# Kernel tuning notes

Hardware: AMD Instinct MI355X
Metric: run time of the kernel (lower is better)

Reference implementation:

```python
import jax, jax.numpy as jnp
import numpy as np

D_IN, D_OUT, K = 128, 256, 16
B, N = 2, 16384
D_HALF = D_OUT // 2
EPS = 1e-6
GROUPS = 16


def conv1x1(x, w, b):
    # x: (B,C,N,K), w: (O,C), b: (O,)
    return jnp.einsum('oc,bcnk->bonk', w, x) + b[None, :, None, None]


def groupnorm(x, w, b, groups=GROUPS):
    Bv, C, Nv, Kv = x.shape
    xr = x.reshape(Bv, groups, C // groups, Nv, Kv)
    m = xr.mean(axis=(2, 3, 4), keepdims=True)
    v = xr.var(axis=(2, 3, 4), keepdims=True)
    xn = ((xr - m) / jnp.sqrt(v + EPS)).reshape(Bv, C, Nv, Kv)
    return xn * w[None, :, None, None] + b[None, :, None, None]


def lse(coords, x, idx, dist, w, b, gw, gb):
    # coords: (B,N,3); x: (B,C,N,1); idx: (B,N,K); dist: (B,N,K)
    nbr = jax.vmap(lambda c, i: c[i])(coords, idx)          # (B,N,K,3)
    ctr = jnp.broadcast_to(coords[:, :, None, :], nbr.shape)  # (B,N,K,3)
    rel = jnp.concatenate([ctr, nbr, ctr - nbr], axis=-1)    # (B,N,K,9)
    geo = jnp.concatenate([rel.transpose(0, 3, 1, 2), dist[:, None, :, :]], axis=1)  # (B,10,N,K)
    geo = jax.nn.relu(groupnorm(conv1x1(geo, w, b), gw, gb))  # (B,d/2,N,K)
    nf = jax.vmap(lambda f, i: f[:, i])(x[..., 0], idx)       # (B,d/2,N,K)
    return jnp.concatenate([geo, nf], axis=1)                 # (B,d,N,K)


def attentive_pool(x, w, b, gw, gb):
    m = x.mean(axis=-1, keepdims=True)  # (B,C,N,1)
    return jax.nn.relu(groupnorm(conv1x1(m, w, b), gw, gb))


def setup_inputs() -> dict:
    key = jax.random.key(0)
    ks = jax.random.split(key, 16)
    s = 0.02
    d = {
        'coords': jax.random.normal(ks[0], (B, N, 3), jnp.float32),
        'features': jax.random.normal(ks[1], (B, D_IN, N, 1), jnp.float32),
        'knn_dist': jax.random.uniform(ks[2], (B, N, K), jnp.float32),
        'knn_idx': jax.random.randint(ks[3], (B, N, K), 0, N),
        'w1': jax.random.normal(ks[4], (D_HALF, D_IN), jnp.float32) * s,
        'b1': jnp.zeros((D_HALF,), jnp.float32),
        'lse1_w': jax.random.normal(ks[5], (D_HALF, 10), jnp.float32) * s,
        'lse1_b': jnp.zeros((D_HALF,), jnp.float32),
        'lse1_gw': jnp.ones((D_HALF,), jnp.float32),
        'lse1_gb': jnp.zeros((D_HALF,), jnp.float32),
        'pool1_w': jax.random.normal(ks[6], (D_HALF, D_OUT), jnp.float32) * s,
        'pool1_b': jnp.zeros((D_HALF,), jnp.float32),
        'pool1_gw': jnp.ones((D_HALF,), jnp.float32),
        'pool1_gb': jnp.zeros((D_HALF,), jnp.float32),
        'lse2_w': jax.random.normal(ks[7], (D_HALF, 10), jnp.float32) * s,
        'lse2_b': jnp.zeros((D_HALF,), jnp.float32),
        'lse2_gw': jnp.ones((D_HALF,), jnp.float32),
        'lse2_gb': jnp.zeros((D_HALF,), jnp.float32),
        'pool2_w': jax.random.normal(ks[8], (D_OUT, D_OUT), jnp.float32) * s,
        'pool2_b': jnp.zeros((D_OUT,), jnp.float32),
        'pool2_gw': jnp.ones((D_OUT,), jnp.float32),
        'pool2_gb': jnp.zeros((D_OUT,), jnp.float32),
        'mlp2_w': jax.random.normal(ks[9], (2 * D_OUT, D_OUT), jnp.float32) * s,
        'mlp2_b': jnp.zeros((2 * D_OUT,), jnp.float32),
        'sc_w': jax.random.normal(ks[10], (2 * D_OUT, D_IN), jnp.float32) * s,
        'sc_b': jnp.zeros((2 * D_OUT,), jnp.float32),
        'sc_gw': jnp.ones((2 * D_OUT,), jnp.float32),
        'sc_gb': jnp.zeros((2 * D_OUT,), jnp.float32),
    }
    return d


def reference(coords, features, knn_dist, knn_idx,
              w1, b1,
              lse1_w, lse1_b, lse1_gw, lse1_gb,
              pool1_w, pool1_b, pool1_gw, pool1_gb,
              lse2_w, lse2_b, lse2_gw, lse2_gb,
              pool2_w, pool2_b, pool2_gw, pool2_gb,
              mlp2_w, mlp2_b, sc_w, sc_b, sc_gw, sc_gb):
    # mlp1: conv + LeakyReLU(0.2), no norm
    x = jax.nn.leaky_relu(conv1x1(features, w1, b1), 0.2)        # (B,d/2,N,1)
    x = lse(coords, x, knn_idx, knn_dist, lse1_w, lse1_b, lse1_gw, lse1_gb)  # (B,d,N,K)
    x = attentive_pool(x, pool1_w, pool1_b, pool1_gw, pool1_gb)  # (B,d/2,N,1)
    x = lse(coords, x, knn_idx, knn_dist, lse2_w, lse2_b, lse2_gw, lse2_gb)  # (B,d,N,K)
    x = attentive_pool(x, pool2_w, pool2_b, pool2_gw, pool2_gb)  # (B,d,N,1)
    main = conv1x1(x, mlp2_w, mlp2_b)                            # (B,2d,N,1)
    short = groupnorm(conv1x1(features, sc_w, sc_b), sc_gw, sc_gb)
    return jax.nn.leaky_relu(main + short, 0.01)                 # (B,2d,N,1)
```

## Files before the change

### kernel.cpp

```cpp
#include <hip/hip_runtime.h>


constexpr int Bc = 2;
constexpr int Nc = 16384;
constexpr int Kc = 16;
constexpr float EPSc = 1e-6f;

typedef __attribute__((ext_vector_type(8))) short short8;
typedef __attribute__((ext_vector_type(4))) short short4v;
typedef __attribute__((ext_vector_type(4))) float floatx4;

__device__ inline short f2bf(float x) {
    union { float f; unsigned u; } v; v.f = x;
    unsigned r = v.u + 0x7fffu + ((v.u >> 16) & 1u);
    return (short)(r >> 16);
}
__device__ inline float bf2f(short s) {
    union { unsigned u; float f; } v;
    v.u = ((unsigned)(unsigned short)s) << 16;
    return v.f;
}

constexpr size_t OW_W1  = 0;
constexpr size_t OW_P1W = OW_W1  + 128*128;
constexpr size_t OW_P2W = OW_P1W + 128*256;
constexpr size_t OW_M2W = OW_P2W + 256*256;
constexpr size_t OW_SCW = OW_M2W + 512*256;
constexpr size_t OW_L1W = OW_SCW + 512*128;
constexpr size_t OW_L2W = OW_L1W + 128*32;
constexpr size_t OW_FB  = OW_L2W + 128*32;
constexpr size_t OW_X1  = OW_FB  + (size_t)Bc*Nc*128;
constexpr size_t OW_M   = OW_X1  + (size_t)Bc*Nc*128;
constexpr size_t OW_Z1  = OW_M   + (size_t)Bc*Nc*256;
constexpr size_t OW_Z2  = OW_Z1  + (size_t)Bc*Nc*128;
constexpr size_t OW_S   = OW_Z2  + (size_t)Bc*Nc*256;

constexpr int CV0 = 128*128;
constexpr int CV1 = CV0 + 128*256;
constexpr int CV2 = CV1 + 256*256;
constexpr int CV3 = CV2 + 512*256;
constexpr int CV4 = CV3 + 512*128;
constexpr int CV5 = CV4 + 128*32;
constexpr int CV6 = CV5 + 128*32;
constexpr int CVTOT = CV6 + 1024;

__global__ void prep_kernel(const float* __restrict__ w1,
                            const float* __restrict__ p1w,
                            const float* __restrict__ p2w,
                            const float* __restrict__ m2w,
                            const float* __restrict__ scw,
                            const float* __restrict__ l1w,
                            const float* __restrict__ l2w,
                            short* __restrict__ W16,
                            float* __restrict__ ST)
{
    int i = blockIdx.x * 256 + threadIdx.x;
    if (i < CV0) { W16[OW_W1  + i] = f2bf(w1[i]); return; }
    if (i < CV1) { int k = i - CV0; W16[OW_P1W + k] = f2bf(p1w[k]); return; }
    if (i < CV2) { int k = i - CV1; W16[OW_P2W + k] = f2bf(p2w[k]); return; }
    if (i < CV3) { int k = i - CV2; W16[OW_M2W + k] = f2bf(m2w[k]); return; }
    if (i < CV4) { int k = i - CV3; W16[OW_SCW + k] = f2bf(scw[k]); return; }
    if (i < CV5) { int k = i - CV4; int o = k >> 5, c = k & 31;
                   W16[OW_L1W + k] = (c < 10) ? f2bf(l1w[o*10+c]) : (short)0; return; }
    if (i < CV6) { int k = i - CV5; int o = k >> 5, c = k & 31;
                   W16[OW_L2W + k] = (c < 10) ? f2bf(l2w[o*10+c]) : (short)0; return; }
    { int k = i - CV6; if (k < 1024) ST[k] = 0.f; }
}

__global__ void feat_t_kernel(const float* __restrict__ in, short* __restrict__ out) {
    int tid  = threadIdx.x;
    int lane = tid & 63, wave = tid >> 6;
    int bb = blockIdx.x / (Nc / 64);
    int n  = (blockIdx.x % (Nc / 64)) * 64 + lane;
    #pragma unroll
    for (int cc = 0; cc < 4; cc++) {
        int c0 = (wave + cc * 4) * 8;
        short8 sv;
        #pragma unroll
        for (int i = 0; i < 8; i++)
            sv[i] = f2bf(in[((size_t)bb * 128 + c0 + i) * Nc + n]);
        *(short8*)&out[((size_t)(bb * Nc + n)) * 128 + c0] = sv;
    }
}

__launch_bounds__(256)
__global__ void geo_reduce_kernel(const float* __restrict__ coords,
                                  const int* __restrict__ knn_idx,
                                  const float* __restrict__ knn_dist,
                                  float* __restrict__ dst)
{
    __shared__ float part[4][65];
    const int tid  = threadIdx.x;
    const int b    = blockIdx.y;
    const int base = blockIdx.x * 256 + tid;
    const float* cb  = coords   + (size_t)b * Nc * 3;
    const int*   ib  = knn_idx  + (size_t)b * Nc * Kc;
    const float* db  = knn_dist + (size_t)b * Nc * Kc;

    float acc[65];
    #pragma unroll
    for (int i = 0; i < 65; i++) acc[i] = 0.f;

    #pragma unroll
    for (int it = 0; it < 4; it++) {
        int r = base + it * 65536;
        int n = r >> 4;
        float cx = cb[n*3+0], cy = cb[n*3+1], cz = cb[n*3+2];
        int   j  = ib[r];
        float nx = cb[j*3+0], ny = cb[j*3+1], nz = cb[j*3+2];
        float d  = db[r];
        float g[10] = {cx,cy,cz,nx,ny,nz,cx-nx,cy-ny,cz-nz,d};
        #pragma unroll
        for (int c = 0; c < 10; c++) acc[c] += g[c];
        int idx = 10;
        #pragma unroll
        for (int c = 0; c < 10; c++)
            #pragma unroll
            for (int c2 = c; c2 < 10; c2++) acc[idx++] += g[c] * g[c2];
    }
    #pragma unroll
    for (int i = 0; i < 65; i++) {
        float v = acc[i];
        #pragma unroll
        for (int off = 1; off < 64; off <<= 1) v += __shfl_xor(v, off);
        acc[i] = v;
    }
    int lane = tid & 63, wave = tid >> 6;
    if (lane == 0) {
        #pragma unroll
        for (int i = 0; i < 65; i++) part[wave][i] = acc[i];
    }
    __syncthreads();
    if (tid < 65) {
        float s = part[0][tid] + part[1][tid] + part[2][tid] + part[3][tid];
        atomicAdd(&dst[b * 65 + tid], s);
    }
}

template<int CIN, int COUT, int GROUP_CH, int MODE>
__launch_bounds__(256)
__global__ void gemm_conv(const short* __restrict__ wA,
                          const short* __restrict__ xB,
                          const float* __restrict__ bias,
                          short* __restrict__ outb,
                          float* __restrict__ outf,
                          float* __restrict__ stats,
                          const short* __restrict__ sbuf,
                          const float* __restrict__ st_sc,
                          const float* __restrict__ gw,
                          const float* __restrict__ gb,
                          float sc_cnt,
                          const float* __restrict__ bst,
                          const float* __restrict__ bgw,
                          const float* __restrict__ bgb,
                          float bcnt)
{
    __shared__ short Abuf[128 * 40];
    __shared__ short Bbuf[128 * 40];
    __shared__ float sstat[32];
    __shared__ float smean[4], sinv[4];
    __shared__ float bsc[256], bsh[256];

    const int tid  = threadIdx.x;
    const int n0   = blockIdx.x * 128;
    const int mo   = blockIdx.y * 128;
    const int b    = blockIdx.z;
    const int lane = tid & 63;
    const int wave = tid >> 6;
    const int wm   = (wave >> 1) * 64;
    const int wn   = (wave & 1) * 64;
    const int l15  = lane & 15;
    const int quad = lane >> 4;

    if constexpr (MODE == 2) { if (tid < 32) sstat[tid] = 0.f; }
    if constexpr (MODE == 3) {
        if (tid < 4) {
            int g = (mo >> 5) + tid;
            float s0 = st_sc[(b * 16 + g) * 2 + 0];
            float s1 = st_sc[(b * 16 + g) * 2 + 1];
            float mean = s0 / sc_cnt;
            float var  = s1 / sc_cnt - mean * mean;
            smean[tid] = mean;
            sinv[tid]  = rsqrtf(var + EPSc);
        }
        if (tid < CIN) {
            int g = tid >> 4;
            float s0 = bst[(b * 16 + g) * 2 + 0];
            float s1 = bst[(b * 16 + g) * 2 + 1];
            float mean = s0 / bcnt;
            float var  = s1 / bcnt - mean * mean;
            float inv  = rsqrtf(var + EPSc);
            float sc_  = inv * bgw[tid];
            bsc[tid] = sc_;
            bsh[tid] = bgb[tid] - mean * sc_;
        }
    }

    floatx4 acc[4][4];
    #pragma unroll
    for (int mi = 0; mi < 4; mi++)
        #pragma unroll
        for (int ni = 0; ni < 4; ni++)
            acc[mi][ni] = (floatx4){0.f, 0.f, 0.f, 0.f};

    const short* wAr = wA + (size_t)mo * CIN;
    const short* xBr = xB + (size_t)b * Nc * CIN + (size_t)n0 * CIN;

    for (int c0 = 0; c0 < CIN; c0 += 32) {
        __syncthreads();
        #pragma unroll
        for (int s = 0; s < 2; s++) {
            int e = tid + s * 256;
            int r = e >> 2, q = e & 3;
            *(short8*)&Abuf[r * 40 + q * 8] =
                *(const short8*)(wAr + (size_t)r * CIN + c0 + q * 8);
            short8 v = *(const short8*)(xBr + (size_t)r * CIN + c0 + q * 8);
            if constexpr (MODE == 3) {
                #pragma unroll
                for (int i = 0; i < 8; i++) {
                    int ch = c0 + q * 8 + i;
                    float t = bf2f(v[i]) * bsc[ch] + bsh[ch];
                    v[i] = f2bf(t > 0.f ? t : 0.f);
                }
            }
            *(short8*)&Bbuf[r * 40 + q * 8] = v;
        }
        __syncthreads();

        short8 af[4], bfr[4];
        #pragma unroll
        for (int mi = 0; mi < 4; mi++)
            af[mi] = *(short8*)&Abuf[(wm + mi * 16 + l15) * 40 + quad * 8];
        #pragma unroll
        for (int ni = 0; ni < 4; ni++)
            bfr[ni] = *(short8*)&Bbuf[(wn + ni * 16 + l15) * 40 + quad * 8];
        #pragma unroll
        for (int mi = 0; mi < 4; mi++)
            #pragma unroll
            for (int ni = 0; ni < 4; ni++)
                acc[mi][ni] = __builtin_amdgcn_mfma_f32_16x16x32_bf16(
                    af[mi], bfr[ni], acc[mi][ni], 0, 0, 0);
    }

    #pragma unroll
    for (int mi = 0; mi < 4; mi++) {
        int rowl = wm + mi * 16 + quad * 4;
        float b4[4], gw4[4], gb4[4];
        #pragma unroll
        for (int r = 0; r < 4; r++) {
            b4[r] = bias[mo + rowl + r];
            if constexpr (MODE == 3) {
                gw4[r] = gw[mo + rowl + r];
                gb4[r] = gb[mo + rowl + r];
            }
        }
        float gs = 0.f, gq = 0.f;
        #pragma unroll
        for (int ni = 0; ni < 4; ni++) {
            int col = n0 + wn + ni * 16 + l15;
            if constexpr (MODE == 3) {
                short4v s4 = *(const short4v*)&sbuf[((size_t)(b * Nc + col)) * 512 + mo + rowl];
                int gl = rowl >> 5;
                #pragma unroll
                for (int r = 0; r < 4; r++) {
                    float v = acc[mi][ni][r] + b4[r];
                    float s = bf2f(s4[r]);
                    float sn = (s - smean[gl]) * sinv[gl] * gw4[r] + gb4[r];
                    float o = v + sn;
                    o = o > 0.f ? o : 0.01f * o;
                    outf[((size_t)b * COUT + mo + rowl + r) * Nc + col] = o;
                }
            } else {
                short4v sv;
                #pragma unroll
                for (int r = 0; r < 4; r++) {
                    float v = acc[mi][ni][r] + b4[r];
                    if constexpr (MODE == 1) v = v > 0.f ? v : 0.2f * v;
                    if constexpr (MODE == 2) { gs += v; gq += v * v; }
                    sv[r] = f2bf(v);
                }
                *(short4v*)&outb[((size_t)(b * Nc + col)) * COUT + mo + rowl] = sv;
            }
        }
        if constexpr (MODE == 2) {
            #pragma unroll
            for (int off = 1; off < 16; off <<= 1) {
                gs += __shfl_xor(gs, off);
                gq += __shfl_xor(gq, off);
            }
            if (l15 == 0) {
                int gl = rowl / GROUP_CH;
                atomicAdd(&sstat[gl * 2 + 0], gs);
                atomicAdd(&sstat[gl * 2 + 1], gq);
            }
        }
    }
    if constexpr (MODE == 2) {
        __syncthreads();
        constexpr int NG = 128 / GROUP_CH;
        if (tid < 2 * NG) {
            int g0 = mo / GROUP_CH;
            atomicAdd(&stats[b * 32 + (g0 + (tid >> 1)) * 2 + (tid & 1)], sstat[tid]);
        }
    }
}

__launch_bounds__(256)
__global__ void lse_m_kernel(const float* __restrict__ coords,
                             const int* __restrict__ knn_idx,
                             const float* __restrict__ knn_dist,
                             const short* __restrict__ xprev,
                             const short* __restrict__ wpad,
                             const float* __restrict__ wf,
                             const float* __restrict__ bias,
                             const float* __restrict__ gw,
                             const float* __restrict__ gb,
                             const float* __restrict__ geoS,
                             const float* __restrict__ xst,
                             const float* __restrict__ xgw,
                             const float* __restrict__ xgb,
                             float xcnt,
                             short* __restrict__ m)
{
    __shared__ short Abuf[128 * 40];
    __shared__ short Bbuf[256 * 40];
    __shared__ int   jl[256];
    __shared__ float osum[128], osq[128];
    __shared__ float smean[16], sinv[16];
    __shared__ float xscs[128], xshs[128];

    const int tid = threadIdx.x;
    const int b   = blockIdx.x >> 10;
    const int n0  = (blockIdx.x & 1023) * 16;
    const float NK = (float)(Nc * Kc);
    const bool norm = (xst != nullptr);

    {
        int* bz = (int*)Bbuf;
        #pragma unroll
        for (int i = 0; i < 20; i++) bz[tid + i * 256] = 0;
    }
    #pragma unroll
    for (int s = 0; s < 2; s++) {
        int e = tid + s * 256;
        int o = e >> 2, q = e & 3;
        *(short8*)&Abuf[o * 40 + q * 8] = *(const short8*)(wpad + o * 32 + q * 8);
    }
    if (tid < 128) {
        const float* S = geoS + b * 65;
        float w[10];
        #pragma unroll
        for (int c = 0; c < 10; c++) w[c] = wf[tid * 10 + c];
        float wS = 0.f;
        #pragma unroll
        for (int c = 0; c < 10; c++) wS += w[c] * S[c];
        float q = 0.f;
        {
            int idx = 10;
            #pragma unroll
            for (int c = 0; c < 10; c++)
                #pragma unroll
                for (int c2 = c; c2 < 10; c2++) {
                    float t = w[c] * w[c2] * S[idx++];
                    q += (c == c2) ? t : 2.f * t;
                }
        }
        float bo = bias[tid];
        osum[tid] = NK * bo + wS;
        osq[tid]  = NK * bo * bo + 2.f * bo * wS + q;
        if (norm) {
            int g = tid >> 3;
            float s0 = xst[(b * 16 + g) * 2 + 0];
            float s1 = xst[(b * 16 + g) * 2 + 1];
            float mean = s0 / xcnt;
            float var  = s1 / xcnt - mean * mean;
            float inv  = rsqrtf(var + EPSc);
            float sc_  = inv * xgw[tid];
            xscs[tid] = sc_;
            xshs[tid] = xgb[tid] - mean * sc_;
        }
    }
    __syncthreads();

    {
        int pt = tid & 15, k = tid >> 4;
        int n  = n0 + pt;
        const float* cb = coords + (size_t)b * Nc * 3;
        float cx = cb[n*3+0], cy = cb[n*3+1], cz = cb[n*3+2];
        int   j  = knn_idx[((size_t)b * Nc + n) * Kc + k];
        float nx = cb[j*3+0], ny = cb[j*3+1], nz = cb[j*3+2];
        float d  = knn_dist[((size_t)b * Nc + n) * Kc + k];
        float g[10] = {cx,cy,cz,nx,ny,nz,cx-nx,cy-ny,cz-nz,d};
        int col = k * 16 + pt;
        #pragma unroll
        for (int c = 0; c < 10; c++) Bbuf[col * 40 + c] = f2bf(g[c]);
        jl[col] = j;
    }
    __syncthreads();
    if (tid < 16) {
        float s = 0.f, q = 0.f;
        #pragma unroll
        for (int i = 0; i < 8; i++) { s += osum[tid * 8 + i]; q += osq[tid * 8 + i]; }
        float cnt  = 8.f * NK;
        float mean = s / cnt;
        float var  = q / cnt - mean * mean;
        smean[tid] = mean;
        sinv[tid]  = rsqrtf(var + EPSc);
    }
    __syncthreads();

    const int lane = tid & 63, wave = tid >> 6;
    const int l15 = lane & 15, quad = lane >> 4;
    short8 bfr[16];
    #pragma unroll
    for (int ni = 0; ni < 16; ni++)
        bfr[ni] = *(short8*)&Bbuf[(ni * 16 + l15) * 40 + quad * 8];
    #pragma unroll
    for (int mt2 = 0; mt2 < 2; mt2++) {
        int mt = wave * 2 + mt2;
        short8 af = *(short8*)&Abuf[(mt * 16 + l15) * 40 + quad * 8];
        floatx4 acc[16];
        #pragma unroll
        for (int ni = 0; ni < 16; ni++) {
            acc[ni] = (floatx4){0.f, 0.f, 0.f, 0.f};
            acc[ni] = __builtin_amdgcn_mfma_f32_16x16x32_bf16(af, bfr[ni], acc[ni], 0, 0, 0);
        }
        short4v sv;
        #pragma unroll
        for (int r = 0; r < 4; r++) {
            int o = mt * 16 + quad * 4 + r;
            int g = o >> 3;
            float mu = smean[g], iv = sinv[g];
            float bo = bias[o], gwo = gw[o], gbo = gb[o];
            float s = 0.f;
            #pragma unroll
            for (int ni = 0; ni < 16; ni++) {
                float v = (acc[ni][r] + bo - mu) * iv * gwo + gbo;
                s += v > 0.f ? v : 0.f;
            }
            sv[r] = f2bf(s * (1.f / 16.f));
        }
        *(short4v*)&m[((size_t)(b * Nc + n0 + l15)) * 256 + mt * 16 + quad * 4] = sv;
    }

    {
        int tp = tid & 15, cs = tid >> 4;
        float sc8[8], sh8[8];
        if (norm) {
            #pragma unroll
            for (int i = 0; i < 8; i++) { sc8[i] = xscs[cs*8+i]; sh8[i] = xshs[cs*8+i]; }
        }
        float acc8[8];
        #pragma unroll
        for (int i = 0; i < 8; i++) acc8[i] = 0.f;
        #pragma unroll
        for (int k = 0; k < 16; k++) {
            int j = jl[k * 16 + tp];
            short8 v = *(const short8*)&xprev[((size_t)(b * Nc + j)) * 128 + cs * 8];
            if (norm) {
                #pragma unroll
                for (int i = 0; i < 8; i++) {
                    float t = bf2f(v[i]) * sc8[i] + sh8[i];
                    acc8[i] += t > 0.f ? t : 0.f;
                }
            } else {
                #pragma unroll
                for (int i = 0; i < 8; i++) acc8[i] += bf2f(v[i]);
            }
        }
        short8 sv;
        #pragma unroll
        for (int i = 0; i < 8; i++) sv[i] = f2bf(acc8[i] * (1.f / 16.f));
        *(short8*)&m[((size_t)(b * Nc + n0 + tp)) * 256 + 128 + cs * 8] = sv;
    }
}

extern "C" void kernel_launch(void* const* d_in, const int* in_sizes, int n_in,
                              void* d_out, int out_size, void* d_ws, size_t ws_size,
                              hipStream_t stream)
{
    const float* coords   = (const float*)d_in[0];
    const float* features = (const float*)d_in[1];
    const float* knn_dist = (const float*)d_in[2];
    const int*   knn_idx  = (const int*)  d_in[3];
    const float* w1       = (const float*)d_in[4];
    const float* b1       = (const float*)d_in[5];
    const float* lse1_w   = (const float*)d_in[6];
    const float* lse1_b   = (const float*)d_in[7];
    const float* lse1_gw  = (const float*)d_in[8];
    const float* lse1_gb  = (const float*)d_in[9];
    const float* pool1_w  = (const float*)d_in[10];
    const float* pool1_b  = (const float*)d_in[11];
    const float* pool1_gw = (const float*)d_in[12];
    const float* pool1_gb = (const float*)d_in[13];
    const float* lse2_w   = (const float*)d_in[14];
    const float* lse2_b   = (const float*)d_in[15];
    const float* lse2_gw  = (const float*)d_in[16];
    const float* lse2_gb  = (const float*)d_in[17];
    const float* pool2_w  = (const float*)d_in[18];
    const float* pool2_b  = (const float*)d_in[19];
    const float* pool2_gw = (const float*)d_in[20];
    const float* pool2_gb = (const float*)d_in[21];
    const float* mlp2_w   = (const float*)d_in[22];
    const float* mlp2_b   = (const float*)d_in[23];
    const float* sc_w     = (const float*)d_in[24];
    const float* sc_b     = (const float*)d_in[25];
    const float* sc_gw    = (const float*)d_in[26];
    const float* sc_gb    = (const float*)d_in[27];
    (void)in_sizes; (void)n_in; (void)out_size; (void)ws_size;

    float* ST = (float*)d_ws;
    float* ST_SC  = ST + 0;
    float* ST_P1  = ST + 64;
    float* ST_P2  = ST + 128;
    float* ST_GEO = ST + 256;
    short* W16 = (short*)(ST + 1024);
    short* W1b  = W16 + OW_W1;
    short* P1Wb = W16 + OW_P1W;
    short* P2Wb = W16 + OW_P2W;
    short* M2Wb = W16 + OW_M2W;
    short* SCWb = W16 + OW_SCW;
    short* L1Wb = W16 + OW_L1W;
    short* L2Wb = W16 + OW_L2W;
    short* FB   = W16 + OW_FB;
    short* X1B  = W16 + OW_X1;
    short* MB   = W16 + OW_M;
    short* Z1   = W16 + OW_Z1;
    short* Z2   = W16 + OW_Z2;
    short* SB   = W16 + OW_S;
    float* out  = (float*)d_out;

    prep_kernel<<<(CVTOT + 255) / 256, 256, 0, stream>>>(
        w1, pool1_w, pool2_w, mlp2_w, sc_w, lse1_w, lse2_w, W16, ST);
    feat_t_kernel<<<Bc * Nc / 64, 256, 0, stream>>>(features, FB);
    geo_reduce_kernel<<<dim3(256, Bc), 256, 0, stream>>>(
        coords, knn_idx, knn_dist, ST_GEO);

    gemm_conv<128,512,32,2><<<dim3(Nc/128, 4, Bc), 256, 0, stream>>>(
        SCWb, FB, sc_b, SB, nullptr, ST_SC, nullptr, nullptr, nullptr, nullptr, 0.f,
        nullptr, nullptr, nullptr, 0.f);
    gemm_conv<128,128,8,1><<<dim3(Nc/128, 1, Bc), 256, 0, stream>>>(
        W1b, FB, b1, X1B, nullptr, nullptr, nullptr, nullptr, nullptr, nullptr, 0.f,
        nullptr, nullptr, nullptr, 0.f);
    lse_m_kernel<<<Bc * Nc / 16, 256, 0, stream>>>(
        coords, knn_idx, knn_dist, X1B, L1Wb, lse1_w, lse1_b, lse1_gw, lse1_gb,
        ST_GEO, nullptr, nullptr, nullptr, 0.f, MB);
    gemm_conv<256,128,8,2><<<dim3(Nc/128, 1, Bc), 256, 0, stream>>>(
        P1Wb, MB, pool1_b, Z1, nullptr, ST_P1, nullptr, nullptr, nullptr, nullptr, 0.f,
        nullptr, nullptr, nullptr, 0.f);
    lse_m_kernel<<<Bc * Nc / 16, 256, 0, stream>>>(
        coords, knn_idx, knn_dist, Z1, L2Wb, lse2_w, lse2_b, lse2_gw, lse2_gb,
        ST_GEO, ST_P1, pool1_gw, pool1_gb, (float)(8 * Nc), MB);
    gemm_conv<256,256,16,2><<<dim3(Nc/128, 2, Bc), 256, 0, stream>>>(
        P2Wb, MB, pool2_b, Z2, nullptr, ST_P2, nullptr, nullptr, nullptr, nullptr, 0.f,
        nullptr, nullptr, nullptr, 0.f);
    gemm_conv<256,512,32,3><<<dim3(Nc/128, 4, Bc), 256, 0, stream>>>(
        M2Wb, Z2, mlp2_b, nullptr, out, nullptr, SB, ST_SC, sc_gw, sc_gb,
        (float)(32 * Nc), ST_P2, pool2_gw, pool2_gb, (float)(16 * Nc));
}
```

Baseline: 350.1 us.

## Fuse attentive-pool conv into LSE kernel, keeping pooled features in LDS

The LSE kernel now keeps each 16-point tile's pooled features (256 channels) in shared memory and runs the pool 1x1 conv with MFMA in the same kernel. It writes the pool output and its groupnorm statistics directly, and the two separate pool GEMM launches are removed. This avoids writing and re-reading the intermediate M buffer and saves two launches. In exchange, pool weights are read from global memory by every 16-point block with no LDS staging and with low reuse per block, and the lse weight tile is also read from global memory instead of LDS.

```diff
diff --git a/kernel.cpp b/kernel.cpp
--- a/kernel.cpp
+++ b/kernel.cpp
@@ -30,8 +30,7 @@
 constexpr size_t OW_L2W = OW_L1W + 128*32;
 constexpr size_t OW_FB  = OW_L2W + 128*32;
 constexpr size_t OW_X1  = OW_FB  + (size_t)Bc*Nc*128;
-constexpr size_t OW_M   = OW_X1  + (size_t)Bc*Nc*128;
-constexpr size_t OW_Z1  = OW_M   + (size_t)Bc*Nc*256;
+constexpr size_t OW_Z1  = OW_X1  + (size_t)Bc*Nc*128;
 constexpr size_t OW_Z2  = OW_Z1  + (size_t)Bc*Nc*128;
 constexpr size_t OW_S   = OW_Z2  + (size_t)Bc*Nc*256;
 
@@ -305,29 +304,34 @@
     }
 }
 
+template<int POOL_COUT, int PGROUP>
 __launch_bounds__(256)
-__global__ void lse_m_kernel(const float* __restrict__ coords,
-                             const int* __restrict__ knn_idx,
-                             const float* __restrict__ knn_dist,
-                             const short* __restrict__ xprev,
-                             const short* __restrict__ wpad,
-                             const float* __restrict__ wf,
-                             const float* __restrict__ bias,
-                             const float* __restrict__ gw,
-                             const float* __restrict__ gb,
-                             const float* __restrict__ geoS,
-                             const float* __restrict__ xst,
-                             const float* __restrict__ xgw,
-                             const float* __restrict__ xgb,
-                             float xcnt,
-                             short* __restrict__ m)
+__global__ void lse_pool_kernel(const float* __restrict__ coords,
+                                const int* __restrict__ knn_idx,
+                                const float* __restrict__ knn_dist,
+                                const short* __restrict__ xprev,
+                                const short* __restrict__ wpad,
+                                const float* __restrict__ wf,
+                                const float* __restrict__ gbias,
+                                const float* __restrict__ ggw,
+                                const float* __restrict__ ggb,
+                                const float* __restrict__ geoS,
+                                const float* __restrict__ xst,
+                                const float* __restrict__ xgw,
+                                const float* __restrict__ xgb,
+                                float xcnt,
+                                const short* __restrict__ pw,
+                                const float* __restrict__ pbias,
+                                float* __restrict__ pstats,
+                                short* __restrict__ z)
 {
-    __shared__ short Abuf[128 * 40];
     __shared__ short Bbuf[256 * 40];
+    __shared__ short Mbuf[16 * 264];
     __shared__ int   jl[256];
     __shared__ float osum[128], osq[128];
     __shared__ float smean[16], sinv[16];
     __shared__ float xscs[128], xshs[128];
+    __shared__ float sstat[32];
 
     const int tid = threadIdx.x;
     const int b   = blockIdx.x >> 10;
@@ -335,16 +339,11 @@
     const float NK = (float)(Nc * Kc);
     const bool norm = (xst != nullptr);
 
+    if (tid < 32) sstat[tid] = 0.f;
     {
         int* bz = (int*)Bbuf;
         #pragma unroll
         for (int i = 0; i < 20; i++) bz[tid + i * 256] = 0;
-    }
-    #pragma unroll
-    for (int s = 0; s < 2; s++) {
-        int e = tid + s * 256;
-        int o = e >> 2, q = e & 3;
-        *(short8*)&Abuf[o * 40 + q * 8] = *(const short8*)(wpad + o * 32 + q * 8);
     }
     if (tid < 128) {
         const float* S = geoS + b * 65;
@@ -365,7 +364,7 @@
                     q += (c == c2) ? t : 2.f * t;
                 }
         }
-        float bo = bias[tid];
+        float bo = gbias[tid];
         osum[tid] = NK * bo + wS;
         osq[tid]  = NK * bo * bo + 2.f * bo * wS + q;
         if (norm) {
@@ -418,7 +417,7 @@
     #pragma unroll
     for (int mt2 = 0; mt2 < 2; mt2++) {
         int mt = wave * 2 + mt2;
-        short8 af = *(short8*)&Abuf[(mt * 16 + l15) * 40 + quad * 8];
+        short8 af = *(const short8*)(wpad + (mt * 16 + l15) * 32 + quad * 8);
         floatx4 acc[16];
         #pragma unroll
         for (int ni = 0; ni < 16; ni++) {
@@ -431,7 +430,7 @@
             int o = mt * 16 + quad * 4 + r;
             int g = o >> 3;
             float mu = smean[g], iv = sinv[g];
-            float bo = bias[o], gwo = gw[o], gbo = gb[o];
+            float bo = gbias[o], gwo = ggw[o], gbo = ggb[o];
             float s = 0.f;
             #pragma unroll
             for (int ni = 0; ni < 16; ni++) {
@@ -440,7 +439,7 @@
             }
             sv[r] = f2bf(s * (1.f / 16.f));
         }
-        *(short4v*)&m[((size_t)(b * Nc + n0 + l15)) * 256 + mt * 16 + quad * 4] = sv;
+        *(short4v*)&Mbuf[l15 * 264 + mt * 16 + quad * 4] = sv;
     }
 
     {
@@ -471,8 +470,50 @@
         short8 sv;
         #pragma unroll
         for (int i = 0; i < 8; i++) sv[i] = f2bf(acc8[i] * (1.f / 16.f));
-        *(short8*)&m[((size_t)(b * Nc + n0 + tp)) * 256 + 128 + cs * 8] = sv;
-    }
+        *(short8*)&Mbuf[tp * 264 + 128 + cs * 8] = sv;
+    }
+    __syncthreads();
+
+    constexpr int MTW = POOL_COUT / 64;
+    floatx4 pacc[MTW];
+    #pragma unroll
+    for (int mi = 0; mi < MTW; mi++) pacc[mi] = (floatx4){0.f, 0.f, 0.f, 0.f};
+    #pragma unroll
+    for (int kc = 0; kc < 8; kc++) {
+        short8 bfp = *(short8*)&Mbuf[l15 * 264 + kc * 32 + quad * 8];
+        #pragma unroll
+        for (int mi = 0; mi < MTW; mi++) {
+            int mt = wave * MTW + mi;
+            short8 afp = *(const short8*)(pw + (size_t)(mt * 16 + l15) * 256 + kc * 32 + quad * 8);
+            pacc[mi] = __builtin_amdgcn_mfma_f32_16x16x32_bf16(afp, bfp, pacc[mi], 0, 0, 0);
+        }
+    }
+    #pragma unroll
+    for (int mi = 0; mi < MTW; mi++) {
+        int mt = wave * MTW + mi;
+        float gs = 0.f, gq = 0.f;
+        short4v sv;
+        #pragma unroll
+        for (int r = 0; r < 4; r++) {
+            int o = mt * 16 + quad * 4 + r;
+            float v = pacc[mi][r] + pbias[o];
+            gs += v; gq += v * v;
+            sv[r] = f2bf(v);
+        }
+        *(short4v*)&z[((size_t)(b * Nc + n0 + l15)) * POOL_COUT + mt * 16 + quad * 4] = sv;
+        #pragma unroll
+        for (int off = 1; off < 16; off <<= 1) {
+            gs += __shfl_xor(gs, off);
+            gq += __shfl_xor(gq, off);
+        }
+        if (l15 == 0) {
+            int g = (mt * 16 + quad * 4) / PGROUP;
+            atomicAdd(&sstat[g * 2 + 0], gs);
+            atomicAdd(&sstat[g * 2 + 1], gq);
+        }
+    }
+    __syncthreads();
+    if (tid < 32) atomicAdd(&pstats[b * 32 + tid], sstat[tid]);
 }
 
 extern "C" void kernel_launch(void* const* d_in, const int* in_sizes, int n_in,
@@ -524,7 +565,6 @@
     short* L2Wb = W16 + OW_L2W;
     short* FB   = W16 + OW_FB;
     short* X1B  = W16 + OW_X1;
-    short* MB   = W16 + OW_M;
     short* Z1   = W16 + OW_Z1;
     short* Z2   = W16 + OW_Z2;
     short* SB   = W16 + OW_S;
@@ -542,18 +582,12 @@
     gemm_conv<128,128,8,1><<<dim3(Nc/128, 1, Bc), 256, 0, stream>>>(
         W1b, FB, b1, X1B, nullptr, nullptr, nullptr, nullptr, nullptr, nullptr, 0.f,
         nullptr, nullptr, nullptr, 0.f);
-    lse_m_kernel<<<Bc * Nc / 16, 256, 0, stream>>>(
+    lse_pool_kernel<128,8><<<Bc * Nc / 16, 256, 0, stream>>>(
         coords, knn_idx, knn_dist, X1B, L1Wb, lse1_w, lse1_b, lse1_gw, lse1_gb,
-        ST_GEO, nullptr, nullptr, nullptr, 0.f, MB);
-    gemm_conv<256,128,8,2><<<dim3(Nc/128, 1, Bc), 256, 0, stream>>>(
-        P1Wb, MB, pool1_b, Z1, nullptr, ST_P1, nullptr, nullptr, nullptr, nullptr, 0.f,
-        nullptr, nullptr, nullptr, 0.f);
-    lse_m_kernel<<<Bc * Nc / 16, 256, 0, stream>>>(
+        ST_GEO, nullptr, nullptr, nullptr, 0.f, P1Wb, pool1_b, ST_P1, Z1);
+    lse_pool_kernel<256,16><<<Bc * Nc / 16, 256, 0, stream>>>(
         coords, knn_idx, knn_dist, Z1, L2Wb, lse2_w, lse2_b, lse2_gw, lse2_gb,
-        ST_GEO, ST_P1, pool1_gw, pool1_gb, (float)(8 * Nc), MB);
-    gemm_conv<256,256,16,2><<<dim3(Nc/128, 2, Bc), 256, 0, stream>>>(
-        P2Wb, MB, pool2_b, Z2, nullptr, ST_P2, nullptr, nullptr, nullptr, nullptr, 0.f,
-        nullptr, nullptr, nullptr, 0.f);
+        ST_GEO, ST_P1, pool1_gw, pool1_gb, (float)(8 * Nc), P2Wb, pool2_b, ST_P2, Z2);
     gemm_conv<256,512,32,3><<<dim3(Nc/128, 4, Bc), 256, 0, stream>>>(
         M2Wb, Z2, mlp2_b, nullptr, out, nullptr, SB, ST_SC, sc_gw, sc_gb,
         (float)(32 * Nc), ST_P2, pool2_gw, pool2_gb, (float)(16 * Nc));
```

Measured after the change: 370.0 us. +5.7%, slower.

## Fuse shortcut and mlp1 GEMMs; precompute LSE groupnorm params in one kernel

Applied to the files above, without the earlier changes.

Lays SCW and W1 out contiguously in the bf16 weight buffer so one gemm_conv launch (new MODE 4, 5 row tiles) computes both the shortcut conv with its stats and the mlp1 conv with LeakyReLU. A new single-block lse_param_kernel computes the per-channel groupnorm scale and shift for both LSE stages once, instead of every lse_m block redoing it. lse_m_kernel no longer stages weights into shared memory, reads A fragments directly from global, and writes the padded geometry rows as vector stores. This trades one launch and redundant per-block setup for an extra tiny launch and a runtime branch inside the fused GEMM epilogue.

```diff
diff --git a/kernel.cpp b/kernel.cpp
--- a/kernel.cpp
+++ b/kernel.cpp
@@ -21,12 +21,12 @@
     return v.f;
 }
 
-constexpr size_t OW_W1  = 0;
-constexpr size_t OW_P1W = OW_W1  + 128*128;
+constexpr size_t OW_P1W = 0;
 constexpr size_t OW_P2W = OW_P1W + 128*256;
 constexpr size_t OW_M2W = OW_P2W + 256*256;
 constexpr size_t OW_SCW = OW_M2W + 512*256;
-constexpr size_t OW_L1W = OW_SCW + 512*128;
+constexpr size_t OW_W1  = OW_SCW + 512*128;
+constexpr size_t OW_L1W = OW_W1  + 128*128;
 constexpr size_t OW_L2W = OW_L1W + 128*32;
 constexpr size_t OW_FB  = OW_L2W + 128*32;
 constexpr size_t OW_X1  = OW_FB  + (size_t)Bc*Nc*128;
@@ -35,36 +35,36 @@
 constexpr size_t OW_Z2  = OW_Z1  + (size_t)Bc*Nc*128;
 constexpr size_t OW_S   = OW_Z2  + (size_t)Bc*Nc*256;
 
-constexpr int CV0 = 128*128;
-constexpr int CV1 = CV0 + 128*256;
-constexpr int CV2 = CV1 + 256*256;
-constexpr int CV3 = CV2 + 512*256;
-constexpr int CV4 = CV3 + 512*128;
+constexpr int CV0 = 128*256;
+constexpr int CV1 = CV0 + 256*256;
+constexpr int CV2 = CV1 + 512*256;
+constexpr int CV3 = CV2 + 512*128;
+constexpr int CV4 = CV3 + 128*128;
 constexpr int CV5 = CV4 + 128*32;
 constexpr int CV6 = CV5 + 128*32;
-constexpr int CVTOT = CV6 + 1024;
-
-__global__ void prep_kernel(const float* __restrict__ w1,
-                            const float* __restrict__ p1w,
+constexpr int CVTOT = CV6 + 512;
+
+__global__ void prep_kernel(const float* __restrict__ p1w,
                             const float* __restrict__ p2w,
                             const float* __restrict__ m2w,
                             const float* __restrict__ scw,
+                            const float* __restrict__ w1,
                             const float* __restrict__ l1w,
                             const float* __restrict__ l2w,
                             short* __restrict__ W16,
                             float* __restrict__ ST)
 {
     int i = blockIdx.x * 256 + threadIdx.x;
-    if (i < CV0) { W16[OW_W1  + i] = f2bf(w1[i]); return; }
-    if (i < CV1) { int k = i - CV0; W16[OW_P1W + k] = f2bf(p1w[k]); return; }
-    if (i < CV2) { int k = i - CV1; W16[OW_P2W + k] = f2bf(p2w[k]); return; }
-    if (i < CV3) { int k = i - CV2; W16[OW_M2W + k] = f2bf(m2w[k]); return; }
-    if (i < CV4) { int k = i - CV3; W16[OW_SCW + k] = f2bf(scw[k]); return; }
+    if (i < CV0) { W16[OW_P1W + i] = f2bf(p1w[i]); return; }
+    if (i < CV1) { int k = i - CV0; W16[OW_P2W + k] = f2bf(p2w[k]); return; }
+    if (i < CV2) { int k = i - CV1; W16[OW_M2W + k] = f2bf(m2w[k]); return; }
+    if (i < CV3) { int k = i - CV2; W16[OW_SCW + k] = f2bf(scw[k]); return; }
+    if (i < CV4) { int k = i - CV3; W16[OW_W1  + k] = f2bf(w1[k]); return; }
     if (i < CV5) { int k = i - CV4; int o = k >> 5, c = k & 31;
                    W16[OW_L1W + k] = (c < 10) ? f2bf(l1w[o*10+c]) : (short)0; return; }
     if (i < CV6) { int k = i - CV5; int o = k >> 5, c = k & 31;
                    W16[OW_L2W + k] = (c < 10) ? f2bf(l2w[o*10+c]) : (short)0; return; }
-    { int k = i - CV6; if (k < 1024) ST[k] = 0.f; }
+    { int k = i - CV6; if (k < 512) ST[k] = 0.f; }
 }
 
 __global__ void feat_t_kernel(const float* __restrict__ in, short* __restrict__ out) {
@@ -135,6 +135,63 @@
         float s = part[0][tid] + part[1][tid] + part[2][tid] + part[3][tid];
         atomicAdd(&dst[b * 65 + tid], s);
     }
+}
+
+__launch_bounds__(512)
+__global__ void lse_param_kernel(const float* __restrict__ geoS,
+                                 const float* __restrict__ l1w,
+                                 const float* __restrict__ l1b,
+                                 const float* __restrict__ l1gw,
+                                 const float* __restrict__ l1gb,
+                                 const float* __restrict__ l2w,
+                                 const float* __restrict__ l2b,
+                                 const float* __restrict__ l2gw,
+                                 const float* __restrict__ l2gb,
+                                 float* __restrict__ lp)
+{
+    __shared__ float osum[512], osq[512];
+    const int tid = threadIdx.x;
+    const int s = tid >> 8, r = tid & 255, b = r >> 7, o = r & 127;
+    const float* wf = s ? l2w : l1w;
+    const float* bf = s ? l2b : l1b;
+    const float* gwf = s ? l2gw : l1gw;
+    const float* gbf = s ? l2gb : l1gb;
+    const float NK = (float)(Nc * Kc);
+    const float* S = geoS + b * 65;
+
+    float w[10];
+    #pragma unroll
+    for (int c = 0; c < 10; c++) w[c] = wf[o * 10 + c];
+    float wS = 0.f;
+    #pragma unroll
+    for (int c = 0; c < 10; c++) wS += w[c] * S[c];
+    float q = 0.f;
+    {
+        int idx = 10;
+        #pragma unroll
+        for (int c = 0; c < 10; c++)
+            #pragma unroll
+            for (int c2 = c; c2 < 10; c2++) {
+                float t = w[c] * w[c2] * S[idx++];
+                q += (c == c2) ? t : 2.f * t;
+            }
+    }
+    float bo = bf[o];
+    osum[tid] = NK * bo + wS;
+    osq[tid]  = NK * bo * bo + 2.f * bo * wS + q;
+    __syncthreads();
+    int gb0 = tid & ~7;
+    float gs = 0.f, gq = 0.f;
+    #pragma unroll
+    for (int i = 0; i < 8; i++) { gs += osum[gb0 + i]; gq += osq[gb0 + i]; }
+    float cnt  = 8.f * NK;
+    float mean = gs / cnt;
+    float var  = gq / cnt - mean * mean;
+    float iv   = rsqrtf(var + EPSc);
+    float psc  = iv * gwf[o];
+    float psh  = (bo - mean) * psc + gbf[o];
+    lp[s * 512 + b * 256 + o]       = psc;
+    lp[s * 512 + b * 256 + 128 + o] = psh;
 }
 
 template<int CIN, int COUT, int GROUP_CH, int MODE>
@@ -153,7 +210,9 @@
                           const float* __restrict__ bst,
                           const float* __restrict__ bgw,
                           const float* __restrict__ bgb,
-                          float bcnt)
+                          float bcnt,
+                          const float* __restrict__ bias2,
+                          short* __restrict__ outb2)
 {
     __shared__ short Abuf[128 * 40];
     __shared__ short Bbuf[128 * 40];
@@ -171,8 +230,9 @@
     const int wn   = (wave & 1) * 64;
     const int l15  = lane & 15;
     const int quad = lane >> 4;
-
-    if constexpr (MODE == 2) { if (tid < 32) sstat[tid] = 0.f; }
+    const bool sc_tile = (MODE == 4) && (mo < 512);
+
+    if constexpr (MODE == 2 || MODE == 4) { if (tid < 32) sstat[tid] = 0.f; }
     if constexpr (MODE == 3) {
         if (tid < 4) {
             int g = (mo >> 5) + tid;
@@ -248,7 +308,11 @@
         float b4[4], gw4[4], gb4[4];
         #pragma unroll
         for (int r = 0; r < 4; r++) {
-            b4[r] = bias[mo + rowl + r];
+            if constexpr (MODE == 4) {
+                b4[r] = sc_tile ? bias[mo + rowl + r] : bias2[mo - 512 + rowl + r];
+            } else {
+                b4[r] = bias[mo + rowl + r];
+            }
             if constexpr (MODE == 3) {
                 gw4[r] = gw[mo + rowl + r];
                 gb4[r] = gb[mo + rowl + r];
@@ -270,6 +334,19 @@
                     o = o > 0.f ? o : 0.01f * o;
                     outf[((size_t)b * COUT + mo + rowl + r) * Nc + col] = o;
                 }
+            } else if constexpr (MODE == 4) {
+                short4v sv;
+                #pragma unroll
+                for (int r = 0; r < 4; r++) {
+                    float v = acc[mi][ni][r] + b4[r];
+                    if (sc_tile) { gs += v; gq += v * v; }
+                    else v = v > 0.f ? v : 0.2f * v;
+                    sv[r] = f2bf(v);
+                }
+                if (sc_tile)
+                    *(short4v*)&outb[((size_t)(b * Nc + col)) * 512 + mo + rowl] = sv;
+                else
+                    *(short4v*)&outb2[((size_t)(b * Nc + col)) * 128 + mo - 512 + rowl] = sv;
             } else {
                 short4v sv;
                 #pragma unroll
@@ -282,7 +359,7 @@
                 *(short4v*)&outb[((size_t)(b * Nc + col)) * COUT + mo + rowl] = sv;
             }
         }
-        if constexpr (MODE == 2) {
+        if ((MODE == 2) || (MODE == 4 && sc_tile)) {
             #pragma unroll
             for (int off = 1; off < 16; off <<= 1) {
                 gs += __shfl_xor(gs, off);
@@ -295,7 +372,7 @@
             }
         }
     }
-    if constexpr (MODE == 2) {
+    if ((MODE == 2) || (MODE == 4 && sc_tile)) {
         __syncthreads();
         constexpr int NG = 128 / GROUP_CH;
         if (tid < 2 * NG) {
@@ -311,77 +388,33 @@
                              const float* __restrict__ knn_dist,
                              const short* __restrict__ xprev,
                              const short* __restrict__ wpad,
-                             const float* __restrict__ wf,
-                             const float* __restrict__ bias,
-                             const float* __restrict__ gw,
-                             const float* __restrict__ gb,
-                             const float* __restrict__ geoS,
+                             const float* __restrict__ lp,
                              const float* __restrict__ xst,
                              const float* __restrict__ xgw,
                              const float* __restrict__ xgb,
                              float xcnt,
                              short* __restrict__ m)
 {
-    __shared__ short Abuf[128 * 40];
     __shared__ short Bbuf[256 * 40];
     __shared__ int   jl[256];
-    __shared__ float osum[128], osq[128];
-    __shared__ float smean[16], sinv[16];
     __shared__ float xscs[128], xshs[128];
 
     const int tid = threadIdx.x;
     const int b   = blockIdx.x >> 10;
     const int n0  = (blockIdx.x & 1023) * 16;
-    const float NK = (float)(Nc * Kc);
     const bool norm = (xst != nullptr);
 
-    {
-        int* bz = (int*)Bbuf;
-        #pragma unroll
-        for (int i = 0; i < 20; i++) bz[tid + i * 256] = 0;
-    }
-    #pragma unroll
-    for (int s = 0; s < 2; s++) {
-        int e = tid + s * 256;
-        int o = e >> 2, q = e & 3;
-        *(short8*)&Abuf[o * 40 + q * 8] = *(const short8*)(wpad + o * 32 + q * 8);
-    }
-    if (tid < 128) {
-        const float* S = geoS + b * 65;
-        float w[10];
-        #pragma unroll
-        for (int c = 0; c < 10; c++) w[c] = wf[tid * 10 + c];
-        float wS = 0.f;
-        #pragma unroll
-        for (int c = 0; c < 10; c++) wS += w[c] * S[c];
-        float q = 0.f;
-        {
-            int idx = 10;
-            #pragma unroll
-            for (int c = 0; c < 10; c++)
-                #pragma unroll
-                for (int c2 = c; c2 < 10; c2++) {
-                    float t = w[c] * w[c2] * S[idx++];
-                    q += (c == c2) ? t : 2.f * t;
-                }
-        }
-        float bo = bias[tid];
-        osum[tid] = NK * bo + wS;
-        osq[tid]  = NK * bo * bo + 2.f * bo * wS + q;
-        if (norm) {
-            int g = tid >> 3;
-            float s0 = xst[(b * 16 + g) * 2 + 0];
-            float s1 = xst[(b * 16 + g) * 2 + 1];
-            float mean = s0 / xcnt;
-            float var  = s1 / xcnt - mean * mean;
-            float inv  = rsqrtf(var + EPSc);
-            float sc_  = inv * xgw[tid];
-            xscs[tid] = sc_;
-            xshs[tid] = xgb[tid] - mean * sc_;
-        }
-    }
-    __syncthreads();
-
+    if (norm && tid < 128) {
+        int g = tid >> 3;
+        float s0 = xst[(b * 16 + g) * 2 + 0];
+        float s1 = xst[(b * 16 + g) * 2 + 1];
+        float mean = s0 / xcnt;
+        float var  = s1 / xcnt - mean * mean;
+        float inv  = rsqrtf(var + EPSc);
+        float sc_  = inv * xgw[tid];
+        xscs[tid] = sc_;
+        xshs[tid] = xgb[tid] - mean * sc_;
+    }
     {
         int pt = tid & 15, k = tid >> 4;
         int n  = n0 + pt;
@@ -390,22 +423,21 @@
         int   j  = knn_idx[((size_t)b * Nc + n) * Kc + k];
         float nx = cb[j*3+0], ny = cb[j*3+1], nz = cb[j*3+2];
         float d  = knn_dist[((size_t)b * Nc + n) * Kc + k];
-        float g[10] = {cx,cy,cz,nx,ny,nz,cx-nx,cy-ny,cz-nz,d};
         int col = k * 16 + pt;
-        #pragma unroll
-        for (int c = 0; c < 10; c++) Bbuf[col * 40 + c] = f2bf(g[c]);
+        short8 w0, w1, zz;
+        w0[0]=f2bf(cx); w0[1]=f2bf(cy); w0[2]=f2bf(cz);
+        w0[3]=f2bf(nx); w0[4]=f2bf(ny); w0[5]=f2bf(nz);
+        w0[6]=f2bf(cx-nx); w0[7]=f2bf(cy-ny);
+        w1[0]=f2bf(cz-nz); w1[1]=f2bf(d);
+        #pragma unroll
+        for (int i = 2; i < 8; i++) w1[i] = 0;
+        #pragma unroll
+        for (int i = 0; i < 8; i++) zz[i] = 0;
+        *(short8*)&Bbuf[col * 40 + 0]  = w0;
+        *(short8*)&Bbuf[col * 40 + 8]  = w1;
+        *(short8*)&Bbuf[col * 40 + 16] = zz;
+        *(short8*)&Bbuf[col * 40 + 24] = zz;
         jl[col] = j;
-    }
-    __syncthreads();
-    if (tid < 16) {
-        float s = 0.f, q = 0.f;
-        #pragma unroll
-        for (int i = 0; i < 8; i++) { s += osum[tid * 8 + i]; q += osq[tid * 8 + i]; }
-        float cnt  = 8.f * NK;
-        float mean = s / cnt;
-        float var  = q / cnt - mean * mean;
-        smean[tid] = mean;
-        sinv[tid]  = rsqrtf(var + EPSc);
     }
     __syncthreads();
 
@@ -418,7 +450,7 @@
     #pragma unroll
     for (int mt2 = 0; mt2 < 2; mt2++) {
         int mt = wave * 2 + mt2;
-        short8 af = *(short8*)&Abuf[(mt * 16 + l15) * 40 + quad * 8];
+        short8 af = *(const short8*)(wpad + (mt * 16 + l15) * 32 + quad * 8);
         floatx4 acc[16];
         #pragma unroll
         for (int ni = 0; ni < 16; ni++) {
@@ -429,13 +461,12 @@
         #pragma unroll
         for (int r = 0; r < 4; r++) {
             int o = mt * 16 + quad * 4 + r;
-            int g = o >> 3;
-            float mu = smean[g], iv = sinv[g];
-            float bo = bias[o], gwo = gw[o], gbo = gb[o];
+            float psc = lp[b * 256 + o];
+            float psh = lp[b * 256 + 128 + o];
             float s = 0.f;
             #pragma unroll
             for (int ni = 0; ni < 16; ni++) {
-                float v = (acc[ni][r] + bo - mu) * iv * gwo + gbo;
+                float v = acc[ni][r] * psc + psh;
                 s += v > 0.f ? v : 0.f;
             }
             sv[r] = f2bf(s * (1.f / 16.f));
@@ -514,8 +545,8 @@
     float* ST_P1  = ST + 64;
     float* ST_P2  = ST + 128;
     float* ST_GEO = ST + 256;
-    short* W16 = (short*)(ST + 1024);
-    short* W1b  = W16 + OW_W1;
+    float* ST_LP  = ST + 512;
+    short* W16 = (short*)(ST + 2048);
     short* P1Wb = W16 + OW_P1W;
     short* P2Wb = W16 + OW_P2W;
     short* M2Wb = W16 + OW_M2W;
@@ -531,30 +562,31 @@
     float* out  = (float*)d_out;
 
     prep_kernel<<<(CVTOT + 255) / 256, 256, 0, stream>>>(
-        w1, pool1_w, pool2_w, mlp2_w, sc_w, lse1_w, lse2_w, W16, ST);
+        pool1_w, pool2_w, mlp2_w, sc_w, w1, lse1_w, lse2_w, W16, ST);
     feat_t_kernel<<<Bc * Nc / 64, 256, 0, stream>>>(features, FB);
     geo_reduce_kernel<<<dim3(256, Bc), 256, 0, stream>>>(
         coords, knn_idx, knn_dist, ST_GEO);
-
-    gemm_conv<128,512,32,2><<<dim3(Nc/128, 4, Bc), 256, 0, stream>>>(
+    lse_param_kernel<<<1, 512, 0, stream>>>(
+        ST_GEO, lse1_w, lse1_b, lse1_gw, lse1_gb,
+        lse2_w, lse2_b, lse2_gw, lse2_gb, ST_LP);
+
+    gemm_conv<128,640,32,4><<<dim3(Nc/128, 5, Bc), 256, 0, stream>>>(
         SCWb, FB, sc_b, SB, nullptr, ST_SC, nullptr, nullptr, nullptr, nullptr, 0.f,
-        nullptr, nullptr, nullptr, 0.f);
-    gemm_conv<128,128,8,1><<<dim3(Nc/128, 1, Bc), 256, 0, stream>>>(
-        W1b, FB, b1, X1B, nullptr, nullptr, nullptr, nullptr, nullptr, nullptr, 0.f,
-        nullptr, nullptr, nullptr, 0.f);
+        nullptr, nullptr, nullptr, 0.f, b1, X1B);
     lse_m_kernel<<<Bc * Nc / 16, 256, 0, stream>>>(
-        coords, knn_idx, knn_dist, X1B, L1Wb, lse1_w, lse1_b, lse1_gw, lse1_gb,
-        ST_GEO, nullptr, nullptr, nullptr, 0.f, MB);
+        coords, knn_idx, knn_dist, X1B, L1Wb, ST_LP,
+        nullptr, nullptr, nullptr, 0.f, MB);
     gemm_conv<256,128,8,2><<<dim3(Nc/128, 1, Bc), 256, 0, stream>>>(
         P1Wb, MB, pool1_b, Z1, nullptr, ST_P1, nullptr, nullptr, nullptr, nullptr, 0.f,
-        nullptr, nullptr, nullptr, 0.f);
+        nullptr, nullptr, nullptr, 0.f, nullptr, nullptr);
     lse_m_kernel<<<Bc * Nc / 16, 256, 0, stream>>>(
-        coords, knn_idx, knn_dist, Z1, L2Wb, lse2_w, lse2_b, lse2_gw, lse2_gb,
-        ST_GEO, ST_P1, pool1_gw, pool1_gb, (float)(8 * Nc), MB);
+        coords, knn_idx, knn_dist, Z1, L2Wb, ST_LP + 512,
+        ST_P1, pool1_gw, pool1_gb, (float)(8 * Nc), MB);
     gemm_conv<256,256,16,2><<<dim3(Nc/128, 2, Bc), 256, 0, stream>>>(
         P2Wb, MB, pool2_b, Z2, nullptr, ST_P2, nullptr, nullptr, nullptr, nullptr, 0.f,
-        nullptr, nullptr, nullptr, 0.f);
+        nullptr, nullptr, nullptr, 0.f, nullptr, nullptr);
     gemm_conv<256,512,32,3><<<dim3(Nc/128, 4, Bc), 256, 0, stream>>>(
         M2Wb, Z2, mlp2_b, nullptr, out, nullptr, SB, ST_SC, sc_gw, sc_gb,
-        (float)(32 * Nc), ST_P2, pool2_gw, pool2_gb, (float)(16 * Nc));
-}
+        (float)(32 * Nc), ST_P2, pool2_gw, pool2_gb, (float)(16 * Nc),
+        nullptr, nullptr);
+}
```

Measured after the change: 334.7 us. -4.4%, faster.
